# Performance work log

Hardware: AMD Instinct MI355X
Metric: run time of the kernel (lower is better)

## Reference

```python
import jax, jax.numpy as jnp
import numpy as np

STEP_PRI = 0.01
STEP_DUAL = 0.01
REG_SP = 0.002
NUM_ITERS = 50
B, N = 512, 64


def _matrix_power(m, p):
    # exponentiation by squaring; p is a static Python int >= 1
    result = jnp.broadcast_to(jnp.eye(m.shape[-1], dtype=m.dtype), m.shape)
    while p > 0:
        if p & 1:
            result = result @ m
        p >>= 1
        if p:
            m = m @ m
    return result


def _matrix_poly(m, d, p):
    # (I + m/d)^p, matching torch matrix_poly
    x = jnp.eye(d, dtype=m.dtype) + m / d
    return _matrix_power(x, p)


def _threshold(x):
    # nn.Threshold(0.5, 0): x if x > 0.5 else 0
    return jnp.where(x > 0.5, x, jnp.zeros_like(x))


def setup_inputs() -> dict:
    key = jax.random.key(0)
    adj = jax.random.uniform(key, (B, N, N), dtype=jnp.float32)
    return {"adj": adj}


def reference(adj):
    n = adj.shape[-1]
    x0 = adj
    scores = _threshold(adj)
    alpha0 = jnp.zeros(adj.shape[0], dtype=adj.dtype)

    def step(carry, _):
        x, alpha = carry
        # grad of augmented Lagrangian (DAG constraint gradient uses (I + x*x/n)^(n-1)^T)
        poly_t = jnp.swapaxes(_matrix_poly(x * x, n, n - 1), -1, -2)
        grad = -scores + 2.0 * alpha[:, None, None] * x * poly_t / n
        til_x = x - STEP_PRI * grad
        # soft-threshold (prox of L1), then clamp to <= 1
        new_x = jax.nn.relu(jnp.abs(til_x) - REG_SP * STEP_PRI)
        x = 1.0 - jax.nn.relu(1.0 - new_x)
        # constraint2: tr((I + x*x/n)^min(30,n)) / n - 1, per batch element
        h = jnp.trace(_matrix_poly(x * x, n, min(30, n)), axis1=-2, axis2=-1) / n - 1.0
        alpha = alpha + STEP_DUAL * h
        return (x, alpha), None

    (x, _), _ = jax.lax.scan(step, (x0, alpha0), None, length=NUM_ITERS)
    return _threshold(x)
```

## Files before the change

### kernel.cpp

```cpp
#include <hip/hip_runtime.h>
#include <stdint.h>

#define PL 4096

typedef unsigned int u32;
typedef unsigned short u16;
typedef float f32x4 __attribute__((ext_vector_type(4)));
typedef short short8 __attribute__((ext_vector_type(8)));

__device__ __forceinline__ u32 prm(u32 a, u32 b, u32 s) {
  return __builtin_amdgcn_perm(a, b, s);
}
__device__ __forceinline__ u32 pk(float f0, float f1) {
  return prm(__float_as_uint(f1), __float_as_uint(f0), 0x07060302u);
}
__device__ __forceinline__ float rlo(u32 w) { return __uint_as_float(w << 16); }
__device__ __forceinline__ float rhi(u32 w) {
  return __uint_as_float(w & 0xffff0000u);
}
__device__ __forceinline__ short8 mk8(u32 w0, u32 w1, u32 w2, u32 w3) {
  union {
    u32 w[4];
    short8 s;
  } u;
  u.w[0] = w0;
  u.w[1] = w1;
  u.w[2] = w2;
  u.w[3] = w3;
  return u.s;
}
__device__ __forceinline__ void dot8(short8 a, short8 b, float& part) {
  union {
    short8 s;
    u32 w[4];
  } ua, ub;
  ua.s = a;
  ub.s = b;
#pragma unroll
  for (int w = 0; w < 4; ++w) {
    part = fmaf(rlo(ua.w[w]), rlo(ub.w[w]), part);
    part = fmaf(rhi(ua.w[w]), rhi(ub.w[w]), part);
  }
}
__device__ __forceinline__ f32x4 MF(short8 a, short8 b, f32x4 c) {
  return __builtin_amdgcn_mfma_f32_16x16x32_bf16(a, b, c, 0, 0, 0);
}

struct AF {
  short8 a0, a1;
};
struct BF8 {
  short8 b[4][2];
};

__device__ __forceinline__ AF macc_to_af(const f32x4 (&m)[4]) {
  u32 P0[4], P1[4];
#pragma unroll
  for (int b = 0; b < 4; ++b) {
    P0[b] = pk(m[b][0], m[b][1]);
    P1[b] = pk(m[b][2], m[b][3]);
  }
  AF r;
  r.a0 = mk8(P0[0], P1[0], P0[1], P1[1]);
  r.a1 = mk8(P0[2], P1[2], P0[3], P1[3]);
  return r;
}

__global__ __launch_bounds__(512, 2) void dag_iter_kernel(
    const float* __restrict__ adj, float* __restrict__ out) {
  __shared__ __align__(16) u16 BUF[6 * PL];
  __shared__ float red[8];

  const int tid = (int)threadIdx.x;
  const int lane = tid & 63;
  const int wv = tid >> 6;
  const int mat = wv >> 2;
  const int w = wv & 3;
  const int l15 = lane & 15;
  const int grp = lane >> 4;
  const int l7 = l15 & 7;

  u16* SM = BUF + mat * 3 * PL;
  u16* P1 = SM + PL;
  u16* P2 = SM + 2 * PL;

  const int c = 16 * w + l15;
  int rb[4][2];
#pragma unroll
  for (int b = 0; b < 4; ++b)
#pragma unroll
    for (int kh = 0; kh < 2; ++kh)
      rb[b][kh] = (16 * b + l15) * 64 + ((((kh << 2) + grp) ^ l7) << 3);
  int sT[4];
#pragma unroll
  for (int b = 0; b < 4; ++b)
    sT[b] = (16 * b + l15) * 64 +
            ((((grp + ((w >> 1) << 2)) ^ ((16 * b + l15) & 7))) << 3) +
            ((w & 1) << 2);
  int stT[2];
#pragma unroll
  for (int h = 0; h < 2; ++h)
    stT[h] = c * 64 + ((((h << 2) + grp) ^ (c & 7)) << 3);

  AF afI;
  {
    const bool mine = (grp == (l15 >> 2));
    const int s = ((w & 1) << 2) + (l15 & 3);
    const u32 onev = (s & 1) ? 0x3F800000u : 0x00003F80u;
    u32 ww[4];
#pragma unroll
    for (int k = 0; k < 4; ++k) ww[k] = (mine && ((s >> 1) == k)) ? onev : 0u;
    short8 hot = mk8(ww[0], ww[1], ww[2], ww[3]);
    short8 zero = mk8(0u, 0u, 0u, 0u);
    afI.a0 = (w < 2) ? hot : zero;
    afI.a1 = (w < 2) ? zero : hot;
  }

  const float* src = adj + (size_t)(2 * blockIdx.x + mat) * 4096;
  float x[4][4], sc[4][4];
#pragma unroll
  for (int b = 0; b < 4; ++b)
#pragma unroll
    for (int j = 0; j < 4; ++j) {
      float v = src[(16 * b + 4 * grp + j) * 64 + c];
      x[b][j] = v;
      sc[b][j] = (v > 0.5f) ? v : 0.0f;
    }
  float alpha = 0.0f;
  AF af;
  AF af3;
  BF8 bf3;
  f32x4 acc63[4];

  auto loadBF = [&](const u16* P) {
    BF8 f;
#pragma unroll
    for (int b = 0; b < 4; ++b) {
      f.b[b][0] = *(const short8*)(P + rb[b][0]);
      f.b[b][1] = *(const short8*)(P + rb[b][1]);
    }
    return f;
  };
  auto mirrorAF = [&](const AF& a, const BF8& bf) {
    const f32x4 Z = {0.0f, 0.0f, 0.0f, 0.0f};
    f32x4 m[4];
    __builtin_amdgcn_s_setprio(1);
#pragma unroll
    for (int b = 0; b < 4; ++b) {
      m[b] = MF(bf.b[b][0], a.a0, Z);
      m[b] = MF(bf.b[b][1], a.a1, m[b]);
    }
    __builtin_amdgcn_s_setprio(0);
    return macc_to_af(m);
  };
  auto primaryT = [&](const AF& a, const BF8& bf, u16* P) {
    const f32x4 Z = {0.0f, 0.0f, 0.0f, 0.0f};
    f32x4 p[4];
    __builtin_amdgcn_s_setprio(1);
#pragma unroll
    for (int b = 0; b < 4; ++b) {
      p[b] = MF(a.a0, bf.b[b][0], Z);
      p[b] = MF(a.a1, bf.b[b][1], p[b]);
    }
    __builtin_amdgcn_s_setprio(0);
#pragma unroll
    for (int b = 0; b < 4; ++b)
      *(uint2*)(P + sT[b]) =
          make_uint2(pk(p[b][0], p[b][1]), pk(p[b][2], p[b][3]));
  };
  auto traceP = [&](const AF& a, const BF8& bf) {
    short8 c0s = bf.b[0][0], c1s = bf.b[0][1];
    if (w == 1) {
      c0s = bf.b[1][0];
      c1s = bf.b[1][1];
    } else if (w == 2) {
      c0s = bf.b[2][0];
      c1s = bf.b[2][1];
    } else if (w == 3) {
      c0s = bf.b[3][0];
      c1s = bf.b[3][1];
    }
    float part = 0.0f;
    dot8(a.a0, c0s, part);
    dot8(a.a1, c1s, part);
#pragma unroll
    for (int off = 1; off < 64; off <<= 1) part += __shfl_xor(part, off);
    if (lane == 0) red[(mat << 2) + w] = part;
  };

  auto prox = [&](float til[4][4]) {
#pragma unroll
    for (int b = 0; b < 4; ++b)
#pragma unroll
      for (int j = 0; j < 4; ++j) {
        float ax = fabsf(til[b][j]) - 2e-5f;
        x[b][j] = fminf(fmaxf(ax, 0.0f), 1.0f);
      }
  };
  auto stageW = [&]() {
    float m[4][4];
#pragma unroll
    for (int b = 0; b < 4; ++b)
#pragma unroll
      for (int j = 0; j < 4; ++j)
        m[b][j] = fmaf(x[b][j] * x[b][j], 0.015625f,
                       (b == w && 4 * grp + j == l15) ? 1.0f : 0.0f);
#pragma unroll
    for (int h = 0; h < 2; ++h)
      *(short8*)(SM + stT[h]) =
          mk8(pk(m[2 * h][0], m[2 * h][1]), pk(m[2 * h][2], m[2 * h][3]),
              pk(m[2 * h + 1][0], m[2 * h + 1][1]),
              pk(m[2 * h + 1][2], m[2 * h + 1][3]));
    __syncthreads();
  };
  auto gradprox = [&]() {
    const int rbase = mat << 2;
    float tr = red[rbase] + red[rbase + 1] + red[rbase + 2] + red[rbase + 3];
    alpha = fmaf(0.01f, tr * 0.015625f - 1.0f, alpha);
    const float a2 = alpha * 0.03125f;
    float til[4][4];
#pragma unroll
    for (int b = 0; b < 4; ++b)
#pragma unroll
      for (int j = 0; j < 4; ++j) {
        float g = fmaf(a2 * x[b][j], acc63[b][j], -sc[b][j]);
        til[b][j] = fmaf(-0.01f, g, x[b][j]);
      }
    prox(til);
  };

  auto segHEAD = [&]() {
    BF8 bm = loadBF(SM);
    AF afm = mirrorAF(afI, bm);
    AF af2 = mirrorAF(afm, bm);
    af3 = mirrorAF(af2, bm);
    primaryT(af2, bm, P1);
    __syncthreads();
  };
  auto segTAIL = [&]() {
    bf3 = loadBF(P1);
    AF af6 = mirrorAF(af3, bf3);
    AF af9 = mirrorAF(af6, bf3);
    AF af12 = mirrorAF(af9, bf3);
    af = mirrorAF(af12, bf3);
    primaryT(af12, bf3, P2);
    __syncthreads();
  };
  auto segFRONT = [&]() {
    BF8 b15 = loadBF(P2);
    traceP(af, b15);
    AF af30 = mirrorAF(af, b15);
    AF af45 = mirrorAF(af30, b15);
    AF af60 = mirrorAF(af45, b15);
    const f32x4 Z = {0.0f, 0.0f, 0.0f, 0.0f};
    __builtin_amdgcn_s_setprio(1);
#pragma unroll
    for (int b = 0; b < 4; ++b) {
      acc63[b] = MF(bf3.b[b][0], af60.a0, Z);
      acc63[b] = MF(bf3.b[b][1], af60.a1, acc63[b]);
    }
    __builtin_amdgcn_s_setprio(0);
    __syncthreads();
  };

  if (mat) {
    __builtin_amdgcn_s_barrier();
    __builtin_amdgcn_s_barrier();
  }

  {
    float til[4][4];
#pragma unroll
    for (int b = 0; b < 4; ++b)
#pragma unroll
      for (int j = 0; j < 4; ++j) til[b][j] = fmaf(0.01f, sc[b][j], x[b][j]);
    prox(til);
    stageW();
  }
  segHEAD();
  segTAIL();
  for (int it = 0; it < 48; ++it) {
    segFRONT();
    gradprox();
    stageW();
    segHEAD();
    segTAIL();
  }
  segFRONT();
  gradprox();

  float* dst = out + (size_t)(2 * blockIdx.x + mat) * 4096;
#pragma unroll
  for (int b = 0; b < 4; ++b)
#pragma unroll
    for (int j = 0; j < 4; ++j) {
      float v = x[b][j];
      dst[(16 * b + 4 * grp + j) * 64 + c] = (v > 0.5f) ? v : 0.0f;
    }

  if (mat == 0) {
    __builtin_amdgcn_s_barrier();
    __builtin_amdgcn_s_barrier();
  }
}

extern "C" void kernel_launch(void* const* d_in, const int* in_sizes, int n_in,
                              void* d_out, int out_size, void* d_ws,
                              size_t ws_size, hipStream_t stream) {
  const float* adj = (const float*)d_in[0];
  float* out = (float*)d_out;
  const int nbatch = in_sizes[0] / 4096;
  dag_iter_kernel<<<nbatch / 2, 512, 0, stream>>>(adj, out);
}
```

Measured before the change: 198.6 us.

## Interleave two matrices per wave instead of separate wave groups per matrix

Previously each block ran 512 threads, with two groups of 4 waves each handling one matrix, and staggered barriers were used to offset their phases. Now each block has 4 waves, and each wave processes both matrices with their MFMA chains interleaved. This gives instruction-level parallelism in place of the inter-wave overlap and drops the s_setprio hints. The cost is roughly double the register pressure per wave and fewer waves per CU (launch bounds 256,1), which may reduce latency hiding.

New measurement: 241.3 us. 1.22x slower.

```diff
diff --git a/kernel.cpp b/kernel.cpp
--- a/kernel.cpp
+++ b/kernel.cpp
@@ -66,23 +66,77 @@
   return r;
 }
 
-__global__ __launch_bounds__(512, 2) void dag_iter_kernel(
+__device__ __forceinline__ BF8 loadBF(const u16* __restrict__ P,
+                                      const int (&rb)[4][2]) {
+  BF8 f;
+#pragma unroll
+  for (int b = 0; b < 4; ++b) {
+    f.b[b][0] = *(const short8*)(P + rb[b][0]);
+    f.b[b][1] = *(const short8*)(P + rb[b][1]);
+  }
+  return f;
+}
+
+__device__ __forceinline__ AF mirrorAF(const AF& a, const BF8& bf) {
+  const f32x4 Z = {0.0f, 0.0f, 0.0f, 0.0f};
+  f32x4 m[4];
+#pragma unroll
+  for (int b = 0; b < 4; ++b) {
+    m[b] = MF(bf.b[b][0], a.a0, Z);
+    m[b] = MF(bf.b[b][1], a.a1, m[b]);
+  }
+  return macc_to_af(m);
+}
+
+__device__ __forceinline__ void primaryT(const AF& a, const BF8& bf,
+                                         u16* __restrict__ P,
+                                         const int (&sT)[4]) {
+  const f32x4 Z = {0.0f, 0.0f, 0.0f, 0.0f};
+#pragma unroll
+  for (int b = 0; b < 4; ++b) {
+    f32x4 p = MF(a.a0, bf.b[b][0], Z);
+    p = MF(a.a1, bf.b[b][1], p);
+    *(uint2*)(P + sT[b]) = make_uint2(pk(p[0], p[1]), pk(p[2], p[3]));
+  }
+}
+
+__device__ __forceinline__ float tracePart(const AF& a, const BF8& bf, int w) {
+  short8 c0s = bf.b[0][0], c1s = bf.b[0][1];
+  if (w == 1) {
+    c0s = bf.b[1][0];
+    c1s = bf.b[1][1];
+  } else if (w == 2) {
+    c0s = bf.b[2][0];
+    c1s = bf.b[2][1];
+  } else if (w == 3) {
+    c0s = bf.b[3][0];
+    c1s = bf.b[3][1];
+  }
+  float part = 0.0f;
+  dot8(a.a0, c0s, part);
+  dot8(a.a1, c1s, part);
+#pragma unroll
+  for (int off = 1; off < 64; off <<= 1) part += __shfl_xor(part, off);
+  return part;
+}
+
+__global__ __launch_bounds__(256, 1) void dag_iter_kernel(
     const float* __restrict__ adj, float* __restrict__ out) {
   __shared__ __align__(16) u16 BUF[6 * PL];
   __shared__ float red[8];
+  u16* SM0 = BUF;
+  u16* P10 = BUF + PL;
+  u16* P20 = BUF + 2 * PL;
+  u16* SM1 = BUF + 3 * PL;
+  u16* P11 = BUF + 4 * PL;
+  u16* P21 = BUF + 5 * PL;
 
   const int tid = (int)threadIdx.x;
   const int lane = tid & 63;
-  const int wv = tid >> 6;
-  const int mat = wv >> 2;
-  const int w = wv & 3;
+  const int w = tid >> 6;
   const int l15 = lane & 15;
   const int grp = lane >> 4;
   const int l7 = l15 & 7;
-
-  u16* SM = BUF + mat * 3 * PL;
-  u16* P1 = SM + PL;
-  u16* P2 = SM + 2 * PL;
 
   const int c = 16 * w + l15;
   int rb[4][2];
@@ -116,192 +170,159 @@
     afI.a1 = (w < 2) ? zero : hot;
   }
 
-  const float* src = adj + (size_t)(2 * blockIdx.x + mat) * 4096;
-  float x[4][4], sc[4][4];
+  const float* src0 = adj + (size_t)(2 * blockIdx.x) * 4096;
+  const float* src1 = adj + (size_t)(2 * blockIdx.x + 1) * 4096;
+  float x0[4][4], sc0[4][4], x1[4][4], sc1[4][4];
 #pragma unroll
   for (int b = 0; b < 4; ++b)
 #pragma unroll
     for (int j = 0; j < 4; ++j) {
-      float v = src[(16 * b + 4 * grp + j) * 64 + c];
-      x[b][j] = v;
-      sc[b][j] = (v > 0.5f) ? v : 0.0f;
+      const int off = (16 * b + 4 * grp + j) * 64 + c;
+      float v0 = src0[off];
+      float v1 = src1[off];
+      x0[b][j] = v0;
+      sc0[b][j] = (v0 > 0.5f) ? v0 : 0.0f;
+      x1[b][j] = v1;
+      sc1[b][j] = (v1 > 0.5f) ? v1 : 0.0f;
     }
-  float alpha = 0.0f;
-  AF af;
-  AF af3;
-  BF8 bf3;
-  f32x4 acc63[4];
-
-  auto loadBF = [&](const u16* P) {
-    BF8 f;
-#pragma unroll
-    for (int b = 0; b < 4; ++b) {
-      f.b[b][0] = *(const short8*)(P + rb[b][0]);
-      f.b[b][1] = *(const short8*)(P + rb[b][1]);
-    }
-    return f;
-  };
-  auto mirrorAF = [&](const AF& a, const BF8& bf) {
-    const f32x4 Z = {0.0f, 0.0f, 0.0f, 0.0f};
-    f32x4 m[4];
-    __builtin_amdgcn_s_setprio(1);
-#pragma unroll
-    for (int b = 0; b < 4; ++b) {
-      m[b] = MF(bf.b[b][0], a.a0, Z);
-      m[b] = MF(bf.b[b][1], a.a1, m[b]);
-    }
-    __builtin_amdgcn_s_setprio(0);
-    return macc_to_af(m);
-  };
-  auto primaryT = [&](const AF& a, const BF8& bf, u16* P) {
-    const f32x4 Z = {0.0f, 0.0f, 0.0f, 0.0f};
-    f32x4 p[4];
-    __builtin_amdgcn_s_setprio(1);
-#pragma unroll
-    for (int b = 0; b < 4; ++b) {
-      p[b] = MF(a.a0, bf.b[b][0], Z);
-      p[b] = MF(a.a1, bf.b[b][1], p[b]);
-    }
-    __builtin_amdgcn_s_setprio(0);
-#pragma unroll
-    for (int b = 0; b < 4; ++b)
-      *(uint2*)(P + sT[b]) =
-          make_uint2(pk(p[b][0], p[b][1]), pk(p[b][2], p[b][3]));
-  };
-  auto traceP = [&](const AF& a, const BF8& bf) {
-    short8 c0s = bf.b[0][0], c1s = bf.b[0][1];
-    if (w == 1) {
-      c0s = bf.b[1][0];
-      c1s = bf.b[1][1];
-    } else if (w == 2) {
-      c0s = bf.b[2][0];
-      c1s = bf.b[2][1];
-    } else if (w == 3) {
-      c0s = bf.b[3][0];
-      c1s = bf.b[3][1];
-    }
-    float part = 0.0f;
-    dot8(a.a0, c0s, part);
-    dot8(a.a1, c1s, part);
-#pragma unroll
-    for (int off = 1; off < 64; off <<= 1) part += __shfl_xor(part, off);
-    if (lane == 0) red[(mat << 2) + w] = part;
-  };
-
-  auto prox = [&](float til[4][4]) {
+  float alpha0 = 0.0f, alpha1 = 0.0f;
+  AF af0, af1;
+  BF8 bf3_0, bf3_1;
+  f32x4 a63_0[4], a63_1[4];
+
+  auto proxOne = [&](const float (&til)[4][4], float (&xx)[4][4]) {
 #pragma unroll
     for (int b = 0; b < 4; ++b)
 #pragma unroll
       for (int j = 0; j < 4; ++j) {
         float ax = fabsf(til[b][j]) - 2e-5f;
-        x[b][j] = fminf(fmaxf(ax, 0.0f), 1.0f);
+        xx[b][j] = fminf(fmaxf(ax, 0.0f), 1.0f);
       }
   };
-  auto stageW = [&]() {
+  auto gradproxOne = [&](float (&xx)[4][4], const float (&scc)[4][4],
+                         float& al, const f32x4 (&a63)[4], int rbase) {
+    float tr = red[rbase] + red[rbase + 1] + red[rbase + 2] + red[rbase + 3];
+    al = fmaf(0.01f, tr * 0.015625f - 1.0f, al);
+    const float a2 = al * 0.03125f;
+    float til[4][4];
+#pragma unroll
+    for (int b = 0; b < 4; ++b)
+#pragma unroll
+      for (int j = 0; j < 4; ++j) {
+        float g = fmaf(a2 * xx[b][j], a63[b][j], -scc[b][j]);
+        til[b][j] = fmaf(-0.01f, g, xx[b][j]);
+      }
+    proxOne(til, xx);
+  };
+  auto stageOne = [&](const float (&xx)[4][4], u16* SMp) {
     float m[4][4];
 #pragma unroll
     for (int b = 0; b < 4; ++b)
 #pragma unroll
       for (int j = 0; j < 4; ++j)
-        m[b][j] = fmaf(x[b][j] * x[b][j], 0.015625f,
+        m[b][j] = fmaf(xx[b][j] * xx[b][j], 0.015625f,
                        (b == w && 4 * grp + j == l15) ? 1.0f : 0.0f);
 #pragma unroll
     for (int h = 0; h < 2; ++h)
-      *(short8*)(SM + stT[h]) =
+      *(short8*)(SMp + stT[h]) =
           mk8(pk(m[2 * h][0], m[2 * h][1]), pk(m[2 * h][2], m[2 * h][3]),
               pk(m[2 * h + 1][0], m[2 * h + 1][1]),
               pk(m[2 * h + 1][2], m[2 * h + 1][3]));
-    __syncthreads();
-  };
-  auto gradprox = [&]() {
-    const int rbase = mat << 2;
-    float tr = red[rbase] + red[rbase + 1] + red[rbase + 2] + red[rbase + 3];
-    alpha = fmaf(0.01f, tr * 0.015625f - 1.0f, alpha);
-    const float a2 = alpha * 0.03125f;
-    float til[4][4];
+  };
+
+  auto segHEADTAIL = [&]() {
+    BF8 bm0 = loadBF(SM0, rb);
+    BF8 bm1 = loadBF(SM1, rb);
+    AF afm0 = mirrorAF(afI, bm0);
+    AF afm1 = mirrorAF(afI, bm1);
+    AF af2_0 = mirrorAF(afm0, bm0);
+    AF af2_1 = mirrorAF(afm1, bm1);
+    AF af3a = mirrorAF(af2_0, bm0);
+    AF af3b = mirrorAF(af2_1, bm1);
+    primaryT(af2_0, bm0, P10, sT);
+    primaryT(af2_1, bm1, P11, sT);
+    __syncthreads();
+    bf3_0 = loadBF(P10, rb);
+    bf3_1 = loadBF(P11, rb);
+    AF af6_0 = mirrorAF(af3a, bf3_0);
+    AF af6_1 = mirrorAF(af3b, bf3_1);
+    AF af9_0 = mirrorAF(af6_0, bf3_0);
+    AF af9_1 = mirrorAF(af6_1, bf3_1);
+    AF af12_0 = mirrorAF(af9_0, bf3_0);
+    AF af12_1 = mirrorAF(af9_1, bf3_1);
+    af0 = mirrorAF(af12_0, bf3_0);
+    af1 = mirrorAF(af12_1, bf3_1);
+    primaryT(af12_0, bf3_0, P20, sT);
+    primaryT(af12_1, bf3_1, P21, sT);
+    __syncthreads();
+  };
+  auto segFRONT = [&]() {
+    BF8 b15_0 = loadBF(P20, rb);
+    BF8 b15_1 = loadBF(P21, rb);
+    float p0 = tracePart(af0, b15_0, w);
+    float p1 = tracePart(af1, b15_1, w);
+    if (lane == 0) {
+      red[w] = p0;
+      red[4 + w] = p1;
+    }
+    __syncthreads();
+    AF af30_0 = mirrorAF(af0, b15_0);
+    AF af30_1 = mirrorAF(af1, b15_1);
+    AF af45_0 = mirrorAF(af30_0, b15_0);
+    AF af45_1 = mirrorAF(af30_1, b15_1);
+    AF af60_0 = mirrorAF(af45_0, b15_0);
+    AF af60_1 = mirrorAF(af45_1, b15_1);
+    const f32x4 Z = {0.0f, 0.0f, 0.0f, 0.0f};
+#pragma unroll
+    for (int b = 0; b < 4; ++b) {
+      a63_0[b] = MF(bf3_0.b[b][0], af60_0.a0, Z);
+      a63_1[b] = MF(bf3_1.b[b][0], af60_1.a0, Z);
+      a63_0[b] = MF(bf3_0.b[b][1], af60_0.a1, a63_0[b]);
+      a63_1[b] = MF(bf3_1.b[b][1], af60_1.a1, a63_1[b]);
+    }
+  };
+
+  {
+    float til0[4][4], til1[4][4];
 #pragma unroll
     for (int b = 0; b < 4; ++b)
 #pragma unroll
       for (int j = 0; j < 4; ++j) {
-        float g = fmaf(a2 * x[b][j], acc63[b][j], -sc[b][j]);
-        til[b][j] = fmaf(-0.01f, g, x[b][j]);
+        til0[b][j] = fmaf(0.01f, sc0[b][j], x0[b][j]);
+        til1[b][j] = fmaf(0.01f, sc1[b][j], x1[b][j]);
       }
-    prox(til);
-  };
-
-  auto segHEAD = [&]() {
-    BF8 bm = loadBF(SM);
-    AF afm = mirrorAF(afI, bm);
-    AF af2 = mirrorAF(afm, bm);
-    af3 = mirrorAF(af2, bm);
-    primaryT(af2, bm, P1);
-    __syncthreads();
-  };
-  auto segTAIL = [&]() {
-    bf3 = loadBF(P1);
-    AF af6 = mirrorAF(af3, bf3);
-    AF af9 = mirrorAF(af6, bf3);
-    AF af12 = mirrorAF(af9, bf3);
-    af = mirrorAF(af12, bf3);
-    primaryT(af12, bf3, P2);
-    __syncthreads();
-  };
-  auto segFRONT = [&]() {
-    BF8 b15 = loadBF(P2);
-    traceP(af, b15);
-    AF af30 = mirrorAF(af, b15);
-    AF af45 = mirrorAF(af30, b15);
-    AF af60 = mirrorAF(af45, b15);
-    const f32x4 Z = {0.0f, 0.0f, 0.0f, 0.0f};
-    __builtin_amdgcn_s_setprio(1);
-#pragma unroll
-    for (int b = 0; b < 4; ++b) {
-      acc63[b] = MF(bf3.b[b][0], af60.a0, Z);
-      acc63[b] = MF(bf3.b[b][1], af60.a1, acc63[b]);
-    }
-    __builtin_amdgcn_s_setprio(0);
-    __syncthreads();
-  };
-
-  if (mat) {
-    __builtin_amdgcn_s_barrier();
-    __builtin_amdgcn_s_barrier();
-  }
-
-  {
-    float til[4][4];
-#pragma unroll
-    for (int b = 0; b < 4; ++b)
-#pragma unroll
-      for (int j = 0; j < 4; ++j) til[b][j] = fmaf(0.01f, sc[b][j], x[b][j]);
-    prox(til);
-    stageW();
-  }
-  segHEAD();
-  segTAIL();
+    proxOne(til0, x0);
+    proxOne(til1, x1);
+    stageOne(x0, SM0);
+    stageOne(x1, SM1);
+    __syncthreads();
+    segHEADTAIL();
+  }
   for (int it = 0; it < 48; ++it) {
     segFRONT();
-    gradprox();
-    stageW();
-    segHEAD();
-    segTAIL();
+    gradproxOne(x0, sc0, alpha0, a63_0, 0);
+    gradproxOne(x1, sc1, alpha1, a63_1, 4);
+    stageOne(x0, SM0);
+    stageOne(x1, SM1);
+    __syncthreads();
+    segHEADTAIL();
   }
   segFRONT();
-  gradprox();
-
-  float* dst = out + (size_t)(2 * blockIdx.x + mat) * 4096;
+  gradproxOne(x0, sc0, alpha0, a63_0, 0);
+  gradproxOne(x1, sc1, alpha1, a63_1, 4);
+
+  float* dst0 = out + (size_t)(2 * blockIdx.x) * 4096;
+  float* dst1 = out + (size_t)(2 * blockIdx.x + 1) * 4096;
 #pragma unroll
   for (int b = 0; b < 4; ++b)
 #pragma unroll
     for (int j = 0; j < 4; ++j) {
-      float v = x[b][j];
-      dst[(16 * b + 4 * grp + j) * 64 + c] = (v > 0.5f) ? v : 0.0f;
+      const int off = (16 * b + 4 * grp + j) * 64 + c;
+      float v0 = x0[b][j];
+      float v1 = x1[b][j];
+      dst0[off] = (v0 > 0.5f) ? v0 : 0.0f;
+      dst1[off] = (v1 > 0.5f) ? v1 : 0.0f;
     }
-
-  if (mat == 0) {
-    __builtin_amdgcn_s_barrier();
-    __builtin_amdgcn_s_barrier();
-  }
 }
 
 extern "C" void kernel_launch(void* const* d_in, const int* in_sizes, int n_in,
@@ -310,5 +331,5 @@
   const float* adj = (const float*)d_in[0];
   float* out = (float*)d_out;
   const int nbatch = in_sizes[0] / 4096;
-  dag_iter_kernel<<<nbatch / 2, 512, 0, stream>>>(adj, out);
-}
+  dag_iter_kernel<<<nbatch / 2, 256, 0, stream>>>(adj, out);
+}
```
